# Optimization experiments

Measured on AMD Instinct MI355X. Metric: run time of the kernel, lower is better.

The kernel has to match this reference:

```python
import jax, jax.numpy as jnp
import numpy as np

B, S, H, NH, NF = 128, 1024, 768, 8, 8
FUSED = 3 * H + NF  # 2312


def _lin(k, o, i):
    return jax.random.normal(k, (o, i), jnp.float32) * (1.0 / np.sqrt(i))


def setup_inputs() -> dict:
    key = jax.random.key(0)
    ks = jax.random.split(key, 20)
    last_hidden = jax.random.normal(ks[0], (B, S, H), jnp.float32)
    arousal_feats = jax.random.normal(ks[1], (B, NF), jnp.float32)
    sep1 = jax.random.randint(ks[2], (B,), 2, 800)
    sep2 = jnp.minimum(sep1 + jax.random.randint(ks[3], (B,), 2, 200), S - 1)
    return {
        "last_hidden": last_hidden,
        "arousal_feats": arousal_feats,
        "sep1": sep1,
        "sep2": sep2,
        "in_proj_w": _lin(ks[4], 3 * H, H),
        "in_proj_b": jnp.zeros((3 * H,), jnp.float32),
        "out_w": _lin(ks[5], H, H),
        "out_b": jnp.zeros((H,), jnp.float32),
        "ln_g": jnp.ones((NF,), jnp.float32),
        "ln_b": jnp.zeros((NF,), jnp.float32),
        "va_w1": _lin(ks[6], 512, FUSED),
        "va_b1": jnp.zeros((512,), jnp.float32),
        "va_w2": _lin(ks[7], 128, 512),
        "va_b2": jnp.zeros((128,), jnp.float32),
        "va_w3": _lin(ks[8], 2, 128),
        "va_b3": jnp.zeros((2,), jnp.float32),
        "pol_w": _lin(ks[9], 3, FUSED),
        "pol_b": jnp.zeros((3,), jnp.float32),
        "aro_w": _lin(ks[10], 3, FUSED),
        "aro_b": jnp.zeros((3,), jnp.float32),
    }


def reference(last_hidden, arousal_feats, sep1, sep2, in_proj_w, in_proj_b,
              out_w, out_b, ln_g, ln_b, va_w1, va_b1, va_w2, va_b2,
              va_w3, va_b3, pol_w, pol_b, aro_w, aro_b):
    b, s, h = last_hidden.shape
    nh, dh = NH, h // NH
    pos = jnp.arange(s)[None, :]  # [1,S]
    # ragged boundaries -> masks (honors s1>1 / s2>s1+1 fallbacks to CLS token)
    text_mask = jnp.where((sep1 > 1)[:, None], (pos >= 1) & (pos < sep1[:, None]), pos == 0)
    asp_mask = jnp.where((sep2 > sep1 + 1)[:, None], (pos > sep1[:, None]) & (pos < sep2[:, None]), pos == 0)
    amf = asp_mask.astype(last_hidden.dtype)
    asp_query = (last_hidden * amf[..., None]).sum(1) / amf.sum(1)[:, None]  # [B,H]
    # MultiheadAttention with a single query per sample, keys/values masked to text span
    wq, wk, wv = jnp.split(in_proj_w, 3, axis=0)
    bq, bk, bv = jnp.split(in_proj_b, 3)
    q = (asp_query @ wq.T + bq).reshape(b, nh, dh)
    k = (last_hidden @ wk.T + bk).reshape(b, s, nh, dh)
    v = (last_hidden @ wv.T + bv).reshape(b, s, nh, dh)
    scale = 1.0 / np.sqrt(dh)
    scores = jnp.einsum('bhd,bshd->bhs', q, k) * scale
    scores = jnp.where(text_mask[:, None, :], scores, -jnp.inf)
    attn = jax.nn.softmax(scores, axis=-1)
    ctx = jnp.einsum('bhs,bshd->bhd', attn, v).reshape(b, h)
    cross = ctx @ out_w.T + out_b  # [B,H]
    # ArousalFeatureNorm ~ LayerNorm over feature dim
    mu = arousal_feats.mean(-1, keepdims=True)
    var = arousal_feats.var(-1, keepdims=True)
    aro_n = (arousal_feats - mu) / jnp.sqrt(var + 1e-5) * ln_g + ln_b
    fused = jnp.concatenate([last_hidden[:, 0], cross, asp_query, aro_n], axis=-1)
    hdn = jax.nn.gelu(fused @ va_w1.T + va_b1, approximate=False)
    hdn = jax.nn.gelu(hdn @ va_w2.T + va_b2, approximate=False)
    va = hdn @ va_w3.T + va_b3
    pol = fused @ pol_w.T + pol_b
    aro = fused @ aro_w.T + aro_b
    return (va, pol, aro)
```

## Files before the change

### kernel.cpp

```cpp
#include <hip/hip_runtime.h>
#include <hip/hip_bf16.h>
#include <math.h>

#define B 128
#define S 1024
#define H 768
#define NH 8
#define DH 96
#define FUSED 2312
#define KSPLIT 19
#define KCHUNK 128
#define NOUT 544
#define ASL 8
#define NSL 8
#define FCH 16
#define SCALE 0.10206207261596575f
#define GELU_C 0.70710678118654752f

__device__ __forceinline__ float dot4(float4 a, float4 b) {
    return a.x * b.x + a.y * b.y + a.z * b.z + a.w * b.w;
}

__device__ __forceinline__ float gelu(float x) {
    return 0.5f * x * (1.0f + erff(x * GELU_C));
}

__global__ void aspq_part_kernel(const float* __restrict__ lh,
                                 const int* __restrict__ sep1,
                                 const int* __restrict__ sep2,
                                 float* __restrict__ aspp) {
    int b = blockIdx.x, z = blockIdx.y, t = threadIdx.x;
    int s1 = sep1[b], s2 = sep2[b];
    int lo, hi;
    if (s2 > s1 + 1) { lo = s1 + 1; hi = s2; } else { lo = 0; hi = 1; }
    const float* base = lh + ((size_t)b * S) * H + 4 * t;
    float4 a = {0.f, 0.f, 0.f, 0.f};
    for (int s = lo + z; s < hi; s += ASL) {
        float4 r = *(const float4*)(base + (size_t)s * H);
        a.x += r.x; a.y += r.y; a.z += r.z; a.w += r.w;
    }
    *(float4*)(aspp + (size_t)z * (B * H) + b * H + 4 * t) = a;
}

__global__ void qu_kernel(const float* __restrict__ aspp,
                          const int* __restrict__ sep1,
                          const int* __restrict__ sep2,
                          const float* __restrict__ wq,
                          const float* __restrict__ bq,
                          const float* __restrict__ wk,
                          float* __restrict__ aspq,
                          float* __restrict__ U) {
    int b = blockIdx.x, h = blockIdx.y, t = threadIdx.x;
    int s1 = sep1[b], s2 = sep2[b];
    int lo, hi;
    if (s2 > s1 + 1) { lo = s1 + 1; hi = s2; } else { lo = 0; hi = 1; }
    float inv = 1.0f / (float)(hi - lo);
    __shared__ float aq[H];
    __shared__ float qh[DH];
    for (int c = t; c < H; c += 256) {
        float a = 0.f;
#pragma unroll
        for (int z = 0; z < ASL; ++z)
            a += aspp[(size_t)z * (B * H) + b * H + c];
        a *= inv;
        aq[c] = a;
        if (h == 0) aspq[b * H + c] = a;
    }
    __syncthreads();
    int wave = t >> 6, lane = t & 63;
#pragma unroll
    for (int i = 0; i < 24; ++i) {
        int d = wave * 24 + i;
        const float* wrow = wq + (size_t)(h * DH + d) * H;
        float a = 0.f;
#pragma unroll
        for (int j = 0; j < H / 64; ++j) a += wrow[lane + 64 * j] * aq[lane + 64 * j];
        for (int off = 32; off; off >>= 1) a += __shfl_xor(a, off);
        if (lane == 0) qh[d] = a + bq[h * DH + d];
    }
    __syncthreads();
    float u0 = 0.f, u1 = 0.f, u2 = 0.f;
    for (int d = 0; d < DH; ++d) {
        const float* wrow = wk + (size_t)(h * DH + d) * H;
        float qd = qh[d];
        u0 += qd * wrow[t];
        u1 += qd * wrow[t + 256];
        u2 += qd * wrow[t + 512];
    }
    float* Ub = U + ((size_t)b * NH + h) * H;
    Ub[t] = u0; Ub[t + 256] = u1; Ub[t + 512] = u2;
}

__global__ __launch_bounds__(512) void flash_kernel(
        const float* __restrict__ lhg,
        const float* __restrict__ U,
        const int* __restrict__ sep1,
        float* __restrict__ Op,
        float* __restrict__ mlb) {
    int b = blockIdx.x, z = blockIdx.y, t = threadIdx.x;
    int wave = t >> 6, lane = t & 63;
    int s1 = sep1[b];
    int tlo = (s1 > 1) ? 1 : 0;
    int thi = (s1 > 1) ? s1 : 1;
    int span = thi - tlo;
    int nrows = (span > z) ? ((span - z - 1) / NSL + 1) : 0;

    __shared__ float lhs[FCH][H];

    const float4* Uh = (const float4*)(U + ((size_t)b * NH + wave) * H);
    float4 u0 = Uh[lane], u1 = Uh[lane + 64], u2 = Uh[lane + 128];
    float4 O0 = {0.f, 0.f, 0.f, 0.f}, O1 = O0, O2 = O0;
    float m = -1e30f, l = 0.f;

    int rid = t >> 5;
    int cid = t & 31;

    for (int j0 = 0; j0 < nrows; j0 += FCH) {
        int nv = min(FCH, nrows - j0);
        if (rid < nv) {
            int sg = tlo + z + NSL * (j0 + rid);
            const float4* row = (const float4*)(lhg + ((size_t)b * S + sg) * H);
            float4* dst = (float4*)lhs[rid];
#pragma unroll
            for (int k = 0; k < 6; ++k) dst[cid + 32 * k] = row[cid + 32 * k];
        }
        __syncthreads();
        for (int r = 0; r < nv; ++r) {
            const float4* xr = (const float4*)lhs[r];
            float4 x0 = xr[lane], x1 = xr[lane + 64], x2 = xr[lane + 128];
            float s = dot4(u0, x0) + dot4(u1, x1) + dot4(u2, x2);
            for (int off = 32; off; off >>= 1) s += __shfl_xor(s, off);
            s *= SCALE;
            if (s <= m) {
                float p = __expf(s - m);
                l += p;
                O0.x += p * x0.x; O0.y += p * x0.y; O0.z += p * x0.z; O0.w += p * x0.w;
                O1.x += p * x1.x; O1.y += p * x1.y; O1.z += p * x1.z; O1.w += p * x1.w;
                O2.x += p * x2.x; O2.y += p * x2.y; O2.z += p * x2.z; O2.w += p * x2.w;
            } else {
                float c = __expf(m - s);
                m = s;
                l = l * c + 1.0f;
                O0.x = O0.x * c + x0.x; O0.y = O0.y * c + x0.y;
                O0.z = O0.z * c + x0.z; O0.w = O0.w * c + x0.w;
                O1.x = O1.x * c + x1.x; O1.y = O1.y * c + x1.y;
                O1.z = O1.z * c + x1.z; O1.w = O1.w * c + x1.w;
                O2.x = O2.x * c + x2.x; O2.y = O2.y * c + x2.y;
                O2.z = O2.z * c + x2.z; O2.w = O2.w * c + x2.w;
            }
        }
        __syncthreads();
    }
    float4* Ob = (float4*)(Op + (((size_t)z * B + b) * NH + wave) * H);
    Ob[lane] = O0; Ob[lane + 64] = O1; Ob[lane + 128] = O2;
    if (lane == 0) {
        float* ml = mlb + ((size_t)z * B + b) * NH * 2;
        ml[2 * wave]     = m;
        ml[2 * wave + 1] = l;
    }
}

__global__ __launch_bounds__(256) void mergectx_kernel(
        const float* __restrict__ Op,
        const float* __restrict__ mlb,
        const float* __restrict__ wv,
        const float* __restrict__ bv,
        const float* __restrict__ out_w,
        float* __restrict__ crossp) {
    int b = blockIdx.x, h = blockIdx.y, t = threadIdx.x;
    __shared__ float wsum[H];
    __shared__ float ctxS[DH];
    __shared__ float Wt2[64][100];

    float M = -1e30f;
#pragma unroll
    for (int z = 0; z < NSL; ++z)
        M = fmaxf(M, mlb[(((size_t)z * B + b) * NH + h) * 2]);
    float wz[NSL], L = 0.f;
#pragma unroll
    for (int z = 0; z < NSL; ++z) {
        const float* ml = mlb + (((size_t)z * B + b) * NH + h) * 2;
        float e = __expf(ml[0] - M);
        wz[z] = e;
        L += e * ml[1];
    }
    float Li = 1.0f / L;
    for (int c = t; c < H; c += 256) {
        float a = 0.f;
#pragma unroll
        for (int z = 0; z < NSL; ++z)
            a += wz[z] * Op[(((size_t)z * B + b) * NH + h) * H + c];
        wsum[c] = a * Li;
    }
    __syncthreads();

    int wave = t >> 6, lane = t & 63;
#pragma unroll
    for (int i = 0; i < 24; ++i) {
        int d = wave * 24 + i;
        const float* wrow = wv + (size_t)(h * DH + d) * H;
        float a = 0.f;
#pragma unroll
        for (int j = 0; j < H / 64; ++j) a += wrow[lane + 64 * j] * wsum[lane + 64 * j];
        for (int off = 32; off; off >>= 1) a += __shfl_xor(a, off);
        if (lane == 0) ctxS[d] = a + bv[h * DH + d];
    }
    __syncthreads();

    int r = t >> 2, sub = t & 3;
    for (int o0 = 0; o0 < H; o0 += 64) {
        for (int i = t; i < 64 * 24; i += 256) {
            int rr = i / 24, c4 = (i % 24) * 4;
            float4 w = *(const float4*)(out_w + (size_t)(o0 + rr) * H + h * DH + c4);
            Wt2[rr][c4] = w.x; Wt2[rr][c4 + 1] = w.y;
            Wt2[rr][c4 + 2] = w.z; Wt2[rr][c4 + 3] = w.w;
        }
        __syncthreads();
        float a = 0.f;
#pragma unroll
        for (int j = 0; j < 24; ++j) {
            int d = sub * 24 + j;
            a += Wt2[r][d] * ctxS[d];
        }
        a += __shfl_xor(a, 1);
        a += __shfl_xor(a, 2);
        if (sub == 0)
            crossp[((size_t)h * B + b) * H + o0 + r] = a;
        __syncthreads();
    }
}

__global__ __launch_bounds__(256) void hdn1_kernel(
        const float* __restrict__ lh,
        const float* __restrict__ crossp,
        const float* __restrict__ out_b,
        const float* __restrict__ aspq,
        const float* __restrict__ aro_f,
        const float* __restrict__ ln_g,
        const float* __restrict__ ln_b,
        const float* __restrict__ va_w1,
        const float* __restrict__ pol_w,
        const float* __restrict__ aro_w,
        float* __restrict__ C) {
    int z = blockIdx.z;
    int n0 = blockIdx.x * 32, m0 = blockIdx.y * 32;
    int kbase = z * KCHUNK;
    __shared__ float As[32][33];
    __shared__ float Ws[32][33];
    int t = threadIdx.x;
    int tx = t & 31, ty = t >> 5;
    int lr = t >> 3, lc = (t & 7) * 4;
    float acc[4] = {0.f, 0.f, 0.f, 0.f};
    for (int k0 = kbase; k0 < kbase + KCHUNK; k0 += 32) {
        {
            int bb = m0 + lr;
            int k = k0 + lc;
            float4 a;
            if (k < 768) {
                a = *(const float4*)(lh + (size_t)bb * S * H + k);
            } else if (k < 1536) {
                int c = k - 768;
                a = *(const float4*)(out_b + c);
#pragma unroll
                for (int hh = 0; hh < NH; ++hh) {
                    float4 p = *(const float4*)(crossp + ((size_t)hh * B + bb) * H + c);
                    a.x += p.x; a.y += p.y; a.z += p.z; a.w += p.w;
                }
            } else if (k < 2304) {
                a = *(const float4*)(aspq + (size_t)bb * H + (k - 1536));
            } else if (k < FUSED) {
                const float* af = aro_f + bb * 8;
                float mu = 0.f;
#pragma unroll
                for (int j = 0; j < 8; ++j) mu += af[j];
                mu *= 0.125f;
                float var = 0.f;
#pragma unroll
                for (int j = 0; j < 8; ++j) { float d = af[j] - mu; var += d * d; }
                var *= 0.125f;
                float rs = rsqrtf(var + 1e-5f);
                int c = k - 2304;
                a.x = (af[c]     - mu) * rs * ln_g[c]     + ln_b[c];
                a.y = (af[c + 1] - mu) * rs * ln_g[c + 1] + ln_b[c + 1];
                a.z = (af[c + 2] - mu) * rs * ln_g[c + 2] + ln_b[c + 2];
                a.w = (af[c + 3] - mu) * rs * ln_g[c + 3] + ln_b[c + 3];
            } else {
                a = {0.f, 0.f, 0.f, 0.f};
            }
            As[lr][lc] = a.x; As[lr][lc + 1] = a.y;
            As[lr][lc + 2] = a.z; As[lr][lc + 3] = a.w;
        }
        {
            int n = n0 + lr;
            int kk = min(k0 + lc, FUSED - 4);
            const float* wrow = va_w1 + (size_t)n * FUSED;
            bool valid = true;
            if (n >= 512) {
                if (n < 515)      wrow = pol_w + (size_t)(n - 512) * FUSED;
                else if (n < 518) wrow = aro_w + (size_t)(n - 515) * FUSED;
                else valid = false;
            }
            float4 w = {0.f, 0.f, 0.f, 0.f};
            if (valid) w = *(const float4*)(wrow + kk);
            Ws[lr][lc] = w.x; Ws[lr][lc + 1] = w.y;
            Ws[lr][lc + 2] = w.z; Ws[lr][lc + 3] = w.w;
        }
        __syncthreads();
#pragma unroll
        for (int kk = 0; kk < 32; ++kk) {
            float wv = Ws[tx][kk];
#pragma unroll
            for (int i = 0; i < 4; ++i)
                acc[i] += As[ty + 8 * i][kk] * wv;
        }
        __syncthreads();
    }
    int n = n0 + tx;
#pragma unroll
    for (int i = 0; i < 4; ++i) {
        int mm = m0 + ty + 8 * i;
        C[(size_t)z * (B * NOUT) + (size_t)mm * NOUT + n] = acc[i];
    }
}

__global__ __launch_bounds__(512) void mlp2_kernel(
        const float* __restrict__ hdn1p,
        const float* __restrict__ va_b1,
        const float* __restrict__ va_w2,
        const float* __restrict__ va_b2,
        const float* __restrict__ va_w3,
        const float* __restrict__ va_b3,
        const float* __restrict__ pol_b,
        const float* __restrict__ aro_b,
        float* __restrict__ out) {
    int b = blockIdx.x, t = threadIdx.x;
    int wave = t >> 6, lane = t & 63;
    __shared__ float hsS[512];
    __shared__ float h2S[128];
    {
        float s = 0.f;
#pragma unroll
        for (int z = 0; z < KSPLIT; ++z)
            s += hdn1p[(size_t)z * (B * NOUT) + (size_t)b * NOUT + t];
        hsS[t] = gelu(s + va_b1[t]);
    }
    if (t < 6) {
        float s = 0.f;
#pragma unroll
        for (int z = 0; z < KSPLIT; ++z)
            s += hdn1p[(size_t)z * (B * NOUT) + (size_t)b * NOUT + 512 + t];
        if (t < 3) out[256 + b * 3 + t]       = s + pol_b[t];
        else       out[640 + b * 3 + (t - 3)] = s + aro_b[t - 3];
    }
    __syncthreads();
#pragma unroll
    for (int i = 0; i < 16; ++i) {
        int n = wave * 16 + i;
        float a = 0.f;
#pragma unroll
        for (int j = 0; j < 8; ++j) {
            int k = lane + 64 * j;
            a += hsS[k] * va_w2[(size_t)n * 512 + k];
        }
        for (int off = 32; off; off >>= 1) a += __shfl_xor(a, off);
        if (lane == 0) h2S[n] = gelu(a + va_b2[n]);
    }
    __syncthreads();
    if (wave < 2) {
        float a = h2S[lane] * va_w3[wave * 128 + lane]
                + h2S[lane + 64] * va_w3[wave * 128 + lane + 64];
        for (int off = 32; off; off >>= 1) a += __shfl_xor(a, off);
        if (lane == 0) out[b * 2 + wave] = a + va_b3[wave];
    }
}

extern "C" void kernel_launch(void* const* d_in, const int* in_sizes, int n_in,
                              void* d_out, int out_size, void* d_ws, size_t ws_size,
                              hipStream_t stream) {
    const float* lh    = (const float*)d_in[0];
    const float* aro_f = (const float*)d_in[1];
    const int*   sep1  = (const int*)d_in[2];
    const int*   sep2  = (const int*)d_in[3];
    const float* in_w  = (const float*)d_in[4];
    const float* in_b  = (const float*)d_in[5];
    const float* out_w = (const float*)d_in[6];
    const float* out_b = (const float*)d_in[7];
    const float* ln_g  = (const float*)d_in[8];
    const float* ln_b  = (const float*)d_in[9];
    const float* va_w1 = (const float*)d_in[10];
    const float* va_b1 = (const float*)d_in[11];
    const float* va_w2 = (const float*)d_in[12];
    const float* va_b2 = (const float*)d_in[13];
    const float* va_w3 = (const float*)d_in[14];
    const float* va_b3 = (const float*)d_in[15];
    const float* pol_w = (const float*)d_in[16];
    const float* pol_b = (const float*)d_in[17];
    const float* aro_w = (const float*)d_in[18];
    const float* aro_b = (const float*)d_in[19];
    float* out = (float*)d_out;

    float* ws = (float*)d_ws;
    float* aspp   = ws;
    float* aspq   = aspp + ASL * B * H;
    float* Ubuf   = aspq + B * H;
    float* Opb    = Ubuf + B * NH * H;
    float* mlbuf  = Opb + (size_t)NSL * B * NH * H;
    float* crossp = mlbuf + NSL * B * NH * 2;
    float* hdn1p  = crossp + NH * B * H;

    const float* wq = in_w;
    const float* wk = in_w + H * H;
    const float* wv = in_w + 2 * H * H;
    const float* bq = in_b;
    const float* bv = in_b + 2 * H;

    aspq_part_kernel<<<dim3(B, ASL), 192, 0, stream>>>(lh, sep1, sep2, aspp);
    qu_kernel<<<dim3(B, NH), 256, 0, stream>>>(aspp, sep1, sep2, wq, bq, wk,
                                               aspq, Ubuf);
    flash_kernel<<<dim3(B, NSL), 512, 0, stream>>>(lh, Ubuf, sep1, Opb, mlbuf);
    mergectx_kernel<<<dim3(B, NH), 256, 0, stream>>>(Opb, mlbuf, wv, bv,
                                                     out_w, crossp);
    hdn1_kernel<<<dim3(NOUT / 32, 4, KSPLIT), 256, 0, stream>>>(
        lh, crossp, out_b, aspq, aro_f, ln_g, ln_b,
        va_w1, pol_w, aro_w, hdn1p);
    mlp2_kernel<<<B, 512, 0, stream>>>(hdn1p, va_b1, va_w2, va_b2,
                                       va_w3, va_b3, pol_b, aro_b, out);
}
```

Measured before the change: 262.6 us.

## Fold out_proj into va_w1 weights and co-schedule independent GEMM tiles with attention

Precomputes M = W1_cross · out_w, with out_b folded in as an extra column, in the same launch as the aspect-query partial sums. This removes the per-head out-projection inside mergectx, and the cross part of hdn1 becomes a GEMM over ctx against M. The hdn1 K-chunks that do not depend on ctx run as extra blocks inside the flash-attention launch, so they overlap with attention. The ctx-dependent chunk runs after mergectx in a small split-K GEMM. The price is a weight-weight product computed on every call and half-idle 512-thread GEMM blocks.

```diff
diff --git a/kernel.cpp b/kernel.cpp
--- a/kernel.cpp
+++ b/kernel.cpp
@@ -8,38 +8,109 @@
 #define NH 8
 #define DH 96
 #define FUSED 2312
-#define KSPLIT 19
 #define KCHUNK 128
 #define NOUT 544
+#define MD 800
+#define NZ_NOCTX 13
+#define NZ_CTX 5
+#define NZTOT 18
 #define ASL 8
 #define NSL 8
 #define FCH 16
 #define SCALE 0.10206207261596575f
 #define GELU_C 0.70710678118654752f
 
+#define MTILES (17 * 25)
+#define HTILES (NZ_NOCTX * 4 * 17)
+
 __device__ __forceinline__ float dot4(float4 a, float4 b) {
     return a.x * b.x + a.y * b.y + a.z * b.z + a.w * b.w;
 }
-
 __device__ __forceinline__ float gelu(float x) {
     return 0.5f * x * (1.0f + erff(x * GELU_C));
 }
 
-__global__ void aspq_part_kernel(const float* __restrict__ lh,
-                                 const int* __restrict__ sep1,
-                                 const int* __restrict__ sep2,
-                                 float* __restrict__ aspp) {
-    int b = blockIdx.x, z = blockIdx.y, t = threadIdx.x;
-    int s1 = sep1[b], s2 = sep2[b];
-    int lo, hi;
-    if (s2 > s1 + 1) { lo = s1 + 1; hi = s2; } else { lo = 0; hi = 1; }
-    const float* base = lh + ((size_t)b * S) * H + 4 * t;
-    float4 a = {0.f, 0.f, 0.f, 0.f};
-    for (int s = lo + z; s < hi; s += ASL) {
-        float4 r = *(const float4*)(base + (size_t)s * H);
-        a.x += r.x; a.y += r.y; a.z += r.z; a.w += r.w;
-    }
-    *(float4*)(aspp + (size_t)z * (B * H) + b * H + 4 * t) = a;
+__device__ __forceinline__ const float* wrow_sel(int n, const float* va_w1,
+                                                 const float* pol_w,
+                                                 const float* aro_w,
+                                                 bool& valid) {
+    valid = true;
+    if (n < 512) return va_w1 + (size_t)n * FUSED;
+    if (n < 515) return pol_w + (size_t)(n - 512) * FUSED;
+    if (n < 518) return aro_w + (size_t)(n - 515) * FUSED;
+    valid = false;
+    return va_w1;
+}
+
+__global__ __launch_bounds__(256) void k1_aspq_m(
+        const float* __restrict__ lh,
+        const int* __restrict__ sep1,
+        const int* __restrict__ sep2,
+        const float* __restrict__ va_w1,
+        const float* __restrict__ pol_w,
+        const float* __restrict__ aro_w,
+        const float* __restrict__ out_w,
+        const float* __restrict__ out_b,
+        float* __restrict__ aspp,
+        float* __restrict__ Mbuf) {
+    int bid = blockIdx.x, t = threadIdx.x;
+    if (bid < B * ASL) {
+        if (t >= 192) return;
+        int b = bid >> 3, z = bid & 7;
+        int s1 = sep1[b], s2 = sep2[b];
+        int lo, hi;
+        if (s2 > s1 + 1) { lo = s1 + 1; hi = s2; } else { lo = 0; hi = 1; }
+        const float* base = lh + ((size_t)b * S) * H + 4 * t;
+        float4 a = {0.f, 0.f, 0.f, 0.f};
+        for (int s = lo + z; s < hi; s += ASL) {
+            float4 r = *(const float4*)(base + (size_t)s * H);
+            a.x += r.x; a.y += r.y; a.z += r.z; a.w += r.w;
+        }
+        *(float4*)(aspp + (size_t)z * (B * H) + b * H + 4 * t) = a;
+        return;
+    }
+    int j = bid - B * ASL;
+    int n0 = (j / 25) * 32, d0 = (j % 25) * 32;
+    __shared__ float As[32][33];
+    __shared__ float Ws[32][33];
+    int tx = t & 31, ty = t >> 5;
+    int lr = t >> 3, lc = (t & 7) * 4;
+    float acc[4] = {0.f, 0.f, 0.f, 0.f};
+    for (int k0 = 0; k0 < H; k0 += 32) {
+        {
+            int n = n0 + lr;
+            bool valid;
+            const float* wr = wrow_sel(n, va_w1, pol_w, aro_w, valid);
+            float4 a = {0.f, 0.f, 0.f, 0.f};
+            if (valid) a = *(const float4*)(wr + H + k0 + lc);
+            As[lr][lc] = a.x; As[lr][lc + 1] = a.y;
+            As[lr][lc + 2] = a.z; As[lr][lc + 3] = a.w;
+        }
+        {
+            int c = k0 + lr;
+            float4 w;
+            if (d0 < H) {
+                w = *(const float4*)(out_w + (size_t)c * H + d0 + lc);
+            } else {
+                w.x = (lc == 0) ? out_b[c] : 0.f;
+                w.y = 0.f; w.z = 0.f; w.w = 0.f;
+            }
+            Ws[lc][lr] = w.x; Ws[lc + 1][lr] = w.y;
+            Ws[lc + 2][lr] = w.z; Ws[lc + 3][lr] = w.w;
+        }
+        __syncthreads();
+#pragma unroll
+        for (int kk = 0; kk < 32; ++kk) {
+            float wv = Ws[tx][kk];
+#pragma unroll
+            for (int i = 0; i < 4; ++i)
+                acc[i] += As[ty + 8 * i][kk] * wv;
+        }
+        __syncthreads();
+    }
+#pragma unroll
+    for (int i = 0; i < 4; ++i)
+        Mbuf[(size_t)(n0 + ty + 8 * i) * MD + d0 + tx] = acc[i];
 }
 
 __global__ void qu_kernel(const float* __restrict__ aspp,
@@ -91,149 +162,10 @@
     Ub[t] = u0; Ub[t + 256] = u1; Ub[t + 512] = u2;
 }
 
-__global__ __launch_bounds__(512) void flash_kernel(
+__global__ __launch_bounds__(512) void k3_flash_hdn1(
         const float* __restrict__ lhg,
         const float* __restrict__ U,
         const int* __restrict__ sep1,
-        float* __restrict__ Op,
-        float* __restrict__ mlb) {
-    int b = blockIdx.x, z = blockIdx.y, t = threadIdx.x;
-    int wave = t >> 6, lane = t & 63;
-    int s1 = sep1[b];
-    int tlo = (s1 > 1) ? 1 : 0;
-    int thi = (s1 > 1) ? s1 : 1;
-    int span = thi - tlo;
-    int nrows = (span > z) ? ((span - z - 1) / NSL + 1) : 0;
-
-    __shared__ float lhs[FCH][H];
-
-    const float4* Uh = (const float4*)(U + ((size_t)b * NH + wave) * H);
-    float4 u0 = Uh[lane], u1 = Uh[lane + 64], u2 = Uh[lane + 128];
-    float4 O0 = {0.f, 0.f, 0.f, 0.f}, O1 = O0, O2 = O0;
-    float m = -1e30f, l = 0.f;
-
-    int rid = t >> 5;
-    int cid = t & 31;
-
-    for (int j0 = 0; j0 < nrows; j0 += FCH) {
-        int nv = min(FCH, nrows - j0);
-        if (rid < nv) {
-            int sg = tlo + z + NSL * (j0 + rid);
-            const float4* row = (const float4*)(lhg + ((size_t)b * S + sg) * H);
-            float4* dst = (float4*)lhs[rid];
-#pragma unroll
-            for (int k = 0; k < 6; ++k) dst[cid + 32 * k] = row[cid + 32 * k];
-        }
-        __syncthreads();
-        for (int r = 0; r < nv; ++r) {
-            const float4* xr = (const float4*)lhs[r];
-            float4 x0 = xr[lane], x1 = xr[lane + 64], x2 = xr[lane + 128];
-            float s = dot4(u0, x0) + dot4(u1, x1) + dot4(u2, x2);
-            for (int off = 32; off; off >>= 1) s += __shfl_xor(s, off);
-            s *= SCALE;
-            if (s <= m) {
-                float p = __expf(s - m);
-                l += p;
-                O0.x += p * x0.x; O0.y += p * x0.y; O0.z += p * x0.z; O0.w += p * x0.w;
-                O1.x += p * x1.x; O1.y += p * x1.y; O1.z += p * x1.z; O1.w += p * x1.w;
-                O2.x += p * x2.x; O2.y += p * x2.y; O2.z += p * x2.z; O2.w += p * x2.w;
-            } else {
-                float c = __expf(m - s);
-                m = s;
-                l = l * c + 1.0f;
-                O0.x = O0.x * c + x0.x; O0.y = O0.y * c + x0.y;
-                O0.z = O0.z * c + x0.z; O0.w = O0.w * c + x0.w;
-                O1.x = O1.x * c + x1.x; O1.y = O1.y * c + x1.y;
-                O1.z = O1.z * c + x1.z; O1.w = O1.w * c + x1.w;
-                O2.x = O2.x * c + x2.x; O2.y = O2.y * c + x2.y;
-                O2.z = O2.z * c + x2.z; O2.w = O2.w * c + x2.w;
-            }
-        }
-        __syncthreads();
-    }
-    float4* Ob = (float4*)(Op + (((size_t)z * B + b) * NH + wave) * H);
-    Ob[lane] = O0; Ob[lane + 64] = O1; Ob[lane + 128] = O2;
-    if (lane == 0) {
-        float* ml = mlb + ((size_t)z * B + b) * NH * 2;
-        ml[2 * wave]     = m;
-        ml[2 * wave + 1] = l;
-    }
-}
-
-__global__ __launch_bounds__(256) void mergectx_kernel(
-        const float* __restrict__ Op,
-        const float* __restrict__ mlb,
-        const float* __restrict__ wv,
-        const float* __restrict__ bv,
-        const float* __restrict__ out_w,
-        float* __restrict__ crossp) {
-    int b = blockIdx.x, h = blockIdx.y, t = threadIdx.x;
-    __shared__ float wsum[H];
-    __shared__ float ctxS[DH];
-    __shared__ float Wt2[64][100];
-
-    float M = -1e30f;
-#pragma unroll
-    for (int z = 0; z < NSL; ++z)
-        M = fmaxf(M, mlb[(((size_t)z * B + b) * NH + h) * 2]);
-    float wz[NSL], L = 0.f;
-#pragma unroll
-    for (int z = 0; z < NSL; ++z) {
-        const float* ml = mlb + (((size_t)z * B + b) * NH + h) * 2;
-        float e = __expf(ml[0] - M);
-        wz[z] = e;
-        L += e * ml[1];
-    }
-    float Li = 1.0f / L;
-    for (int c = t; c < H; c += 256) {
-        float a = 0.f;
-#pragma unroll
-        for (int z = 0; z < NSL; ++z)
-            a += wz[z] * Op[(((size_t)z * B + b) * NH + h) * H + c];
-        wsum[c] = a * Li;
-    }
-    __syncthreads();
-
-    int wave = t >> 6, lane = t & 63;
-#pragma unroll
-    for (int i = 0; i < 24; ++i) {
-        int d = wave * 24 + i;
-        const float* wrow = wv + (size_t)(h * DH + d) * H;
-        float a = 0.f;
-#pragma unroll
-        for (int j = 0; j < H / 64; ++j) a += wrow[lane + 64 * j] * wsum[lane + 64 * j];
-        for (int off = 32; off; off >>= 1) a += __shfl_xor(a, off);
-        if (lane == 0) ctxS[d] = a + bv[h * DH + d];
-    }
-    __syncthreads();
-
-    int r = t >> 2, sub = t & 3;
-    for (int o0 = 0; o0 < H; o0 += 64) {
-        for (int i = t; i < 64 * 24; i += 256) {
-            int rr = i / 24, c4 = (i % 24) * 4;
-            float4 w = *(const float4*)(out_w + (size_t)(o0 + rr) * H + h * DH + c4);
-            Wt2[rr][c4] = w.x; Wt2[rr][c4 + 1] = w.y;
-            Wt2[rr][c4 + 2] = w.z; Wt2[rr][c4 + 3] = w.w;
-        }
-        __syncthreads();
-        float a = 0.f;
-#pragma unroll
-        for (int j = 0; j < 24; ++j) {
-            int d = sub * 24 + j;
-            a += Wt2[r][d] * ctxS[d];
-        }
-        a += __shfl_xor(a, 1);
-        a += __shfl_xor(a, 2);
-        if (sub == 0)
-            crossp[((size_t)h * B + b) * H + o0 + r] = a;
-        __syncthreads();
-    }
-}
-
-__global__ __launch_bounds__(256) void hdn1_kernel(
-        const float* __restrict__ lh,
-        const float* __restrict__ crossp,
-        const float* __restrict__ out_b,
         const float* __restrict__ aspq,
         const float* __restrict__ aro_f,
         const float* __restrict__ ln_g,
@@ -241,42 +173,103 @@
         const float* __restrict__ va_w1,
         const float* __restrict__ pol_w,
         const float* __restrict__ aro_w,
-        float* __restrict__ C) {
-    int z = blockIdx.z;
-    int n0 = blockIdx.x * 32, m0 = blockIdx.y * 32;
+        float* __restrict__ Op,
+        float* __restrict__ mlb,
+        float* __restrict__ hdn1p) {
+    __shared__ float smem[FCH * H];
+    int bid = blockIdx.x, t = threadIdx.x;
+
+    if (bid < B * NSL) {
+        int b = bid >> 3, z = bid & 7;
+        int wave = t >> 6, lane = t & 63;
+        int s1 = sep1[b];
+        int tlo = (s1 > 1) ? 1 : 0;
+        int thi = (s1 > 1) ? s1 : 1;
+        int span = thi - tlo;
+        int nrows = (span > z) ? ((span - z - 1) / NSL + 1) : 0;
+        float (*lhs)[H] = (float(*)[H])smem;
+
+        const float4* Uh = (const float4*)(U + ((size_t)b * NH + wave) * H);
+        float4 u0 = Uh[lane], u1 = Uh[lane + 64], u2 = Uh[lane + 128];
+        float4 O0 = {0.f, 0.f, 0.f, 0.f}, O1 = O0, O2 = O0;
+        float m = -1e30f, l = 0.f;
+        int rid = t >> 5, cid = t & 31;
+
+        for (int j0 = 0; j0 < nrows; j0 += FCH) {
+            int nv = min(FCH, nrows - j0);
+            if (rid < nv) {
+                int sg = tlo + z + NSL * (j0 + rid);
+                const float4* row = (const float4*)(lhg + ((size_t)b * S + sg) * H);
+                float4* dst = (float4*)lhs[rid];
+#pragma unroll
+                for (int k = 0; k < 6; ++k) dst[cid + 32 * k] = row[cid + 32 * k];
+            }
+            __syncthreads();
+            for (int r = 0; r < nv; ++r) {
+                const float4* xr = (const float4*)lhs[r];
+                float4 x0 = xr[lane], x1 = xr[lane + 64], x2 = xr[lane + 128];
+                float s = dot4(u0, x0) + dot4(u1, x1) + dot4(u2, x2);
+                for (int off = 32; off; off >>= 1) s += __shfl_xor(s, off);
+                s *= SCALE;
+                if (s <= m) {
+                    float p = __expf(s - m);
+                    l += p;
+                    O0.x += p * x0.x; O0.y += p * x0.y; O0.z += p * x0.z; O0.w += p * x0.w;
+                    O1.x += p * x1.x; O1.y += p * x1.y; O1.z += p * x1.z; O1.w += p * x1.w;
+                    O2.x += p * x2.x; O2.y += p * x2.y; O2.z += p * x2.z; O2.w += p * x2.w;
+                } else {
+                    float c = __expf(m - s);
+                    m = s;
+                    l = l * c + 1.0f;
+                    O0.x = O0.x * c + x0.x; O0.y = O0.y * c + x0.y;
+                    O0.z = O0.z * c + x0.z; O0.w = O0.w * c + x0.w;
+                    O1.x = O1.x * c + x1.x; O1.y = O1.y * c + x1.y;
+                    O1.z = O1.z * c + x1.z; O1.w = O1.w * c + x1.w;
+                    O2.x = O2.x * c + x2.x; O2.y = O2.y * c + x2.y;
+                    O2.z = O2.z * c + x2.z; O2.w = O2.w * c + x2.w;
+                }
+            }
+            __syncthreads();
+        }
+        float4* Ob = (float4*)(Op + (((size_t)z * B + b) * NH + wave) * H);
+        Ob[lane] = O0; Ob[lane + 64] = O1; Ob[lane + 128] = O2;
+        if (lane == 0) {
+            float* ml = mlb + ((size_t)z * B + b) * NH * 2;
+            ml[2 * wave]     = m;
+            ml[2 * wave + 1] = l;
+        }
+        return;
+    }
+
+    int j = bid - B * NSL;
+    int z13 = j / 68, rem = j % 68;
+    int z = (z13 < 6) ? z13 : z13 + 6;
+    int m0 = (rem / 17) * 32, n0 = (rem % 17) * 32;
     int kbase = z * KCHUNK;
-    __shared__ float As[32][33];
-    __shared__ float Ws[32][33];
-    int t = threadIdx.x;
+    float (*As)[33] = (float(*)[33])smem;
+    float (*Ws)[33] = (float(*)[33])(smem + 32 * 33);
     int tx = t & 31, ty = t >> 5;
     int lr = t >> 3, lc = (t & 7) * 4;
     float acc[4] = {0.f, 0.f, 0.f, 0.f};
+    bool active = (t < 256);
     for (int k0 = kbase; k0 < kbase + KCHUNK; k0 += 32) {
-        {
+        if (active) {
             int bb = m0 + lr;
             int k = k0 + lc;
             float4 a;
             if (k < 768) {
-                a = *(const float4*)(lh + (size_t)bb * S * H + k);
-            } else if (k < 1536) {
-                int c = k - 768;
-                a = *(const float4*)(out_b + c);
-#pragma unroll
-                for (int hh = 0; hh < NH; ++hh) {
-                    float4 p = *(const float4*)(crossp + ((size_t)hh * B + bb) * H + c);
-                    a.x += p.x; a.y += p.y; a.z += p.z; a.w += p.w;
-                }
+                a = *(const float4*)(lhg + (size_t)bb * S * H + k);
             } else if (k < 2304) {
                 a = *(const float4*)(aspq + (size_t)bb * H + (k - 1536));
             } else if (k < FUSED) {
                 const float* af = aro_f + bb * 8;
                 float mu = 0.f;
 #pragma unroll
-                for (int j = 0; j < 8; ++j) mu += af[j];
+                for (int jj = 0; jj < 8; ++jj) mu += af[jj];
                 mu *= 0.125f;
                 float var = 0.f;
 #pragma unroll
-                for (int j = 0; j < 8; ++j) { float d = af[j] - mu; var += d * d; }
+                for (int jj = 0; jj < 8; ++jj) { float d = af[jj] - mu; var += d * d; }
                 var *= 0.125f;
                 float rs = rsqrtf(var + 1e-5f);
                 int c = k - 2304;
@@ -289,23 +282,108 @@
             }
             As[lr][lc] = a.x; As[lr][lc + 1] = a.y;
             As[lr][lc + 2] = a.z; As[lr][lc + 3] = a.w;
-        }
-        {
             int n = n0 + lr;
             int kk = min(k0 + lc, FUSED - 4);
-            const float* wrow = va_w1 + (size_t)n * FUSED;
-            bool valid = true;
-            if (n >= 512) {
-                if (n < 515)      wrow = pol_w + (size_t)(n - 512) * FUSED;
-                else if (n < 518) wrow = aro_w + (size_t)(n - 515) * FUSED;
-                else valid = false;
-            }
+            bool valid;
+            const float* wr = wrow_sel(n, va_w1, pol_w, aro_w, valid);
             float4 w = {0.f, 0.f, 0.f, 0.f};
-            if (valid) w = *(const float4*)(wrow + kk);
+            if (valid) w = *(const float4*)(wr + kk);
             Ws[lr][lc] = w.x; Ws[lr][lc + 1] = w.y;
             Ws[lr][lc + 2] = w.z; Ws[lr][lc + 3] = w.w;
         }
         __syncthreads();
+        if (active) {
+#pragma unroll
+            for (int kk = 0; kk < 32; ++kk) {
+                float wv = Ws[tx][kk];
+#pragma unroll
+                for (int i = 0; i < 4; ++i)
+                    acc[i] += As[ty + 8 * i][kk] * wv;
+            }
+        }
+        __syncthreads();
+    }
+    if (active) {
+        int n = n0 + tx;
+#pragma unroll
+        for (int i = 0; i < 4; ++i) {
+            int mm = m0 + ty + 8 * i;
+            hdn1p[(size_t)z13 * (B * NOUT) + (size_t)mm * NOUT + n] = acc[i];
+        }
+    }
+}
+
+__global__ void mergectx_kernel(const float* __restrict__ Op,
+                                const float* __restrict__ mlb,
+                                const float* __restrict__ wv,
+                                const float* __restrict__ bv,
+                                float* __restrict__ ctx) {
+    int b = blockIdx.x, h = blockIdx.y, t = threadIdx.x;
+    float M = -1e30f;
+#pragma unroll
+    for (int z = 0; z < NSL; ++z)
+        M = fmaxf(M, mlb[(((size_t)z * B + b) * NH + h) * 2]);
+    float wz[NSL], L = 0.f;
+#pragma unroll
+    for (int z = 0; z < NSL; ++z) {
+        const float* ml = mlb + (((size_t)z * B + b) * NH + h) * 2;
+        float e = __expf(ml[0] - M);
+        wz[z] = e;
+        L += e * ml[1];
+    }
+    float Li = 1.0f / L;
+    __shared__ float wsum[H];
+    for (int c = t; c < H; c += 256) {
+        float a = 0.f;
+#pragma unroll
+        for (int z = 0; z < NSL; ++z)
+            a += wz[z] * Op[(((size_t)z * B + b) * NH + h) * H + c];
+        wsum[c] = a * Li;
+    }
+    __syncthreads();
+    int wave = t >> 6, lane = t & 63;
+#pragma unroll
+    for (int i = 0; i < 24; ++i) {
+        int d = wave * 24 + i;
+        const float* wrow = wv + (size_t)(h * DH + d) * H;
+        float a = 0.f;
+#pragma unroll
+        for (int j = 0; j < H / 64; ++j) a += wrow[lane + 64 * j] * wsum[lane + 64 * j];
+        for (int off = 32; off; off >>= 1) a += __shfl_xor(a, off);
+        if (lane == 0) ctx[b * H + h * DH + d] = a + bv[h * DH + d];
+    }
+}
+
+__global__ __launch_bounds__(256) void k5_hdn1ctx(
+        const float* __restrict__ ctx,
+        const float* __restrict__ Mbuf,
+        float* __restrict__ hdn1p) {
+    int z = blockIdx.z;
+    int n0 = blockIdx.x * 32, m0 = blockIdx.y * 32;
+    int kbase = z * 160;
+    __shared__ float As[32][33];
+    __shared__ float Ws[32][33];
+    int t = threadIdx.x;
+    int tx = t & 31, ty = t >> 5;
+    int lr = t >> 3, lc = (t & 7) * 4;
+    float acc[4] = {0.f, 0.f, 0.f, 0.f};
+    for (int k0 = kbase; k0 < kbase + 160; k0 += 32) {
+        {
+            int bb = m0 + lr;
+            int k = k0 + lc;
+            float4 a;
+            if (k < 768)      a = *(const float4*)(ctx + (size_t)bb * H + k);
+            else if (k == 768) a = {1.f, 0.f, 0.f, 0.f};
+            else              a = {0.f, 0.f, 0.f, 0.f};
+            As[lr][lc] = a.x; As[lr][lc + 1] = a.y;
+            As[lr][lc + 2] = a.z; As[lr][lc + 3] = a.w;
+        }
+        {
+            float4 w = *(const float4*)(Mbuf + (size_t)(n0 + lr) * MD + k0 + lc);
+            Ws[lr][lc] = w.x; Ws[lr][lc + 1] = w.y;
+            Ws[lr][lc + 2] = w.z; Ws[lr][lc + 3] = w.w;
+        }
+        __syncthreads();
 #pragma unroll
         for (int kk = 0; kk < 32; ++kk) {
             float wv = Ws[tx][kk];
@@ -319,7 +397,7 @@
 #pragma unroll
     for (int i = 0; i < 4; ++i) {
         int mm = m0 + ty + 8 * i;
-        C[(size_t)z * (B * NOUT) + (size_t)mm * NOUT + n] = acc[i];
+        hdn1p[(size_t)(NZ_NOCTX + z) * (B * NOUT) + (size_t)mm * NOUT + n] = acc[i];
     }
 }
 
@@ -340,14 +418,14 @@
     {
         float s = 0.f;
 #pragma unroll
-        for (int z = 0; z < KSPLIT; ++z)
+        for (int z = 0; z < NZTOT; ++z)
             s += hdn1p[(size_t)z * (B * NOUT) + (size_t)b * NOUT + t];
         hsS[t] = gelu(s + va_b1[t]);
     }
     if (t < 6) {
         float s = 0.f;
 #pragma unroll
-        for (int z = 0; z < KSPLIT; ++z)
+        for (int z = 0; z < NZTOT; ++z)
             s += hdn1p[(size_t)z * (B * NOUT) + (size_t)b * NOUT + 512 + t];
         if (t < 3) out[256 + b * 3 + t]       = s + pol_b[t];
         else       out[640 + b * 3 + (t - 3)] = s + aro_b[t - 3];
@@ -405,8 +483,9 @@
     float* Ubuf   = aspq + B * H;
     float* Opb    = Ubuf + B * NH * H;
     float* mlbuf  = Opb + (size_t)NSL * B * NH * H;
-    float* crossp = mlbuf + NSL * B * NH * 2;
-    float* hdn1p  = crossp + NH * B * H;
+    float* ctx    = mlbuf + NSL * B * NH * 2;
+    float* Mbuf   = ctx + B * H;
+    float* hdn1p  = Mbuf + NOUT * MD;
 
     const float* wq = in_w;
     const float* wk = in_w + H * H;
@@ -414,15 +493,15 @@
     const float* bq = in_b;
     const float* bv = in_b + 2 * H;
 
-    aspq_part_kernel<<<dim3(B, ASL), 192, 0, stream>>>(lh, sep1, sep2, aspp);
+    k1_aspq_m<<<B * ASL + MTILES, 256, 0, stream>>>(
+        lh, sep1, sep2, va_w1, pol_w, aro_w, out_w, out_b, aspp, Mbuf);
     qu_kernel<<<dim3(B, NH), 256, 0, stream>>>(aspp, sep1, sep2, wq, bq, wk,
                                                aspq, Ubuf);
-    flash_kernel<<<dim3(B, NSL), 512, 0, stream>>>(lh, Ubuf, sep1, Opb, mlbuf);
-    mergectx_kernel<<<dim3(B, NH), 256, 0, stream>>>(Opb, mlbuf, wv, bv,
-                                                     out_w, crossp);
-    hdn1_kernel<<<dim3(NOUT / 32, 4, KSPLIT), 256, 0, stream>>>(
-        lh, crossp, out_b, aspq, aro_f, ln_g, ln_b,
-        va_w1, pol_w, aro_w, hdn1p);
+    k3_flash_hdn1<<<B * NSL + HTILES, 512, 0, stream>>>(
+        lh, Ubuf, sep1, aspq, aro_f, ln_g, ln_b,
+        va_w1, pol_w, aro_w, Opb, mlbuf, hdn1p);
+    mergectx_kernel<<<dim3(B, NH), 256, 0, stream>>>(Opb, mlbuf, wv, bv, ctx);
+    k5_hdn1ctx<<<dim3(17, 4, NZ_CTX), 256, 0, stream>>>(ctx, Mbuf, hdn1p);
     mlp2_kernel<<<B, 512, 0, stream>>>(hdn1p, va_b1, va_w2, va_b2,
                                        va_w3, va_b3, pol_b, aro_b, out);
 }
```

Measured after the change: 216.0 us. -17.8%, faster.
